# Optimization experiments

Hardware: AMD Instinct MI355X
Metric: run time of the kernel (lower is better)

The kernel has to match this reference:

```python
import jax, jax.numpy as jnp
import numpy as np

BETA = 0.2


def setup_inputs() -> dict:
    key = jax.random.key(0)
    ks = jax.random.split(key, 9)
    B, IN, W, OUT = 1024, 256, 512, 1
    def init_w(k, o, i):
        # torch.nn.Linear default: U(-1/sqrt(in), 1/sqrt(in))
        bound = 1.0 / np.sqrt(i)
        return jax.random.uniform(k, (o, i), jnp.float32, -bound, bound)
    def init_b(k, o, i):
        bound = 1.0 / np.sqrt(i)
        return jax.random.uniform(k, (o,), jnp.float32, -bound, bound)
    return {
        "x":  jax.random.normal(ks[0], (B, IN), jnp.float32),
        "W1": init_w(ks[1], W, IN),  "b1": init_b(ks[2], W, IN),
        "W2": init_w(ks[3], W, W),   "b2": init_b(ks[4], W, W),
        "W3": init_w(ks[5], W, W),   "b3": init_b(ks[6], W, W),
        "W4": init_w(ks[7], OUT, W), "b4": init_b(ks[8], OUT, W),
    }


def _max_tempered_out(x, W, b, beta=BETA):
    # lineared: standard linear part, (B, out)
    lin = jnp.einsum('oi,bi->bo', W, x)
    # tropical part: max over input dim of elementwise weight*input, (B, out)
    mx = jnp.max(W[None, :, :] * x[:, None, :], axis=-1)
    return (1.0 - beta) * lin + beta * mx + b


def reference(x, W1, b1, W2, b2, W3, b3, W4, b4):
    h = _max_tempered_out(x, W1, b1)
    h = _max_tempered_out(h, W2, b2)
    h = _max_tempered_out(h, W3, b3)
    out = _max_tempered_out(h, W4, b4)
    return jnp.squeeze(out, axis=-1)  # output_width == 1 -> (B,)
```

## Files before the change

kernel.cpp:

```cpp
#include <hip/hip_runtime.h>
#include <math.h>


#define NT   512
#define ROWS 4

#define WT1_OFF 0
#define WT2_OFF 33280
#define WT3_OFF 99328

__global__ __launch_bounds__(256) void transpose_all(
    const float* __restrict__ W1, const float* __restrict__ W2,
    const float* __restrict__ W3, float4* __restrict__ ws)
{
    const int tid = blockIdx.x * 256 + threadIdx.x;
    const float* W;
    float4* WT;
    int o, k4, K;
    if (tid < 32768) {
        W = W1; WT = ws + WT1_OFF; K = 256;
        o = tid >> 6; k4 = tid & 63;
    } else if (tid < 98304) {
        const int idx = tid - 32768;
        W = W2; WT = ws + WT2_OFF; K = 512;
        o = idx >> 7; k4 = idx & 127;
    } else {
        const int idx = tid - 98304;
        W = W3; WT = ws + WT3_OFF; K = 512;
        o = idx >> 7; k4 = idx & 127;
    }
    float4 v = *(const float4*)&W[(size_t)o * K + 4 * k4];
    WT[(size_t)k4 * 512 + o] = v;
}

__device__ __forceinline__ void layer_bcast(
    const float (*__restrict__ hin)[512],
    float (*__restrict__ hout)[512],
    const float4* __restrict__ WT,
    const float* __restrict__ bias,
    int K4, int t)
{
    float sa[ROWS], sb[ROWS], ma[ROWS], mb[ROWS];
    #pragma unroll
    for (int r = 0; r < ROWS; ++r) {
        sa[r] = 0.f; sb[r] = 0.f;
        ma[r] = -INFINITY; mb[r] = -INFINITY;
    }

    const float4* wp = WT + t;
    float4 w0 = wp[0];
    float4 w1 = wp[512];
    float4 w2 = wp[1024];
    float4 w3 = wp[1536];

    for (int kg = 0; kg < K4; kg += 4) {
        float4 n0 = w0, n1 = w1, n2 = w2, n3 = w3;
        if (kg + 4 < K4) {
            const float4* q = wp + (size_t)(kg + 4) * 512;
            n0 = q[0];
            n1 = q[512];
            n2 = q[1024];
            n3 = q[1536];
        }
        #pragma unroll
        for (int j = 0; j < 4; ++j) {
            const float4 w = (j == 0) ? w0 : (j == 1) ? w1 : (j == 2) ? w2 : w3;
            const int k = (kg + j) * 4;
            #pragma unroll
            for (int r = 0; r < ROWS; ++r) {
                float4 h = *(const float4*)&hin[r][k];
                float p;
                p = w.x * h.x; sa[r] += p; ma[r] = fmaxf(ma[r], p);
                p = w.y * h.y; sb[r] += p; mb[r] = fmaxf(mb[r], p);
                p = w.z * h.z; sa[r] += p; ma[r] = fmaxf(ma[r], p);
                p = w.w * h.w; sb[r] += p; mb[r] = fmaxf(mb[r], p);
            }
        }
        w0 = n0; w1 = n1; w2 = n2; w3 = n3;
    }

    const float bo = bias[t];
    #pragma unroll
    for (int r = 0; r < ROWS; ++r) {
        float s = sa[r] + sb[r];
        float m = fmaxf(ma[r], mb[r]);
        hout[r][t] = fmaf(0.2f, m, fmaf(0.8f, s, bo));
    }
}

__global__ __launch_bounds__(NT) void net_fused(
    const float* __restrict__ x,
    const float4* __restrict__ WT1, const float* __restrict__ b1,
    const float4* __restrict__ WT2, const float* __restrict__ b2,
    const float4* __restrict__ WT3, const float* __restrict__ b3,
    const float* __restrict__ W4,   const float* __restrict__ b4,
    float* __restrict__ out)
{
    __shared__ __align__(16) float ha[ROWS][512];
    __shared__ __align__(16) float hb[ROWS][512];
    __shared__ float red_s[8][ROWS];
    __shared__ float red_m[8][ROWS];

    const int t = threadIdx.x;
    const int row0 = blockIdx.x * ROWS;

    {
        const int r = t >> 7;
        const int c = (t & 127) * 2;
        float2 v = *(const float2*)&x[(size_t)(row0 + r) * 256 + c];
        ha[r][c]     = v.x;
        ha[r][c + 1] = v.y;
    }
    __syncthreads();

    layer_bcast(ha, hb, WT1, b1, 64,  t);
    __syncthreads();
    layer_bcast(hb, ha, WT2, b2, 128, t);
    __syncthreads();
    layer_bcast(ha, hb, WT3, b3, 128, t);
    __syncthreads();

    const float w4 = W4[t];
    float ps[ROWS], pm[ROWS];
    #pragma unroll
    for (int r = 0; r < ROWS; ++r) {
        float p = w4 * hb[r][t];
        ps[r] = p;
        pm[r] = p;
    }
    #pragma unroll
    for (int off = 32; off; off >>= 1) {
        #pragma unroll
        for (int r = 0; r < ROWS; ++r) {
            ps[r] += __shfl_xor(ps[r], off, 64);
            pm[r] = fmaxf(pm[r], __shfl_xor(pm[r], off, 64));
        }
    }
    const int lane = t & 63;
    const int wave = t >> 6;
    if (lane == 0) {
        #pragma unroll
        for (int r = 0; r < ROWS; ++r) {
            red_s[wave][r] = ps[r];
            red_m[wave][r] = pm[r];
        }
    }
    __syncthreads();

    if (t < ROWS) {
        float s = red_s[0][t];
        float m = red_m[0][t];
        #pragma unroll
        for (int w = 1; w < 8; ++w) {
            s += red_s[w][t];
            m = fmaxf(m, red_m[w][t]);
        }
        out[row0 + t] = fmaf(0.2f, m, fmaf(0.8f, s, b4[0]));
    }
}

extern "C" void kernel_launch(void* const* d_in, const int* in_sizes, int n_in,
                              void* d_out, int out_size, void* d_ws, size_t ws_size,
                              hipStream_t stream)
{
    const float* x  = (const float*)d_in[0];
    const float* W1 = (const float*)d_in[1];
    const float* b1 = (const float*)d_in[2];
    const float* W2 = (const float*)d_in[3];
    const float* b2 = (const float*)d_in[4];
    const float* W3 = (const float*)d_in[5];
    const float* b3 = (const float*)d_in[6];
    const float* W4 = (const float*)d_in[7];
    const float* b4 = (const float*)d_in[8];

    float4* ws4 = (float4*)d_ws;

    transpose_all<<<640, 256, 0, stream>>>(W1, W2, W3, ws4);

    net_fused<<<256, NT, 0, stream>>>(
        x,
        ws4 + WT1_OFF, b1,
        ws4 + WT2_OFF, b2,
        ws4 + WT3_OFF, b3,
        W4, b4,
        (float*)d_out);
}
```

Measured before the change: 66.27 us.

## Deepen weight prefetch, software-pipeline LDS loads, use packed FP32 math

New measurement: 183.9 us. 177% more time.

```diff
diff --git a/kernel.cpp b/kernel.cpp
--- a/kernel.cpp
+++ b/kernel.cpp
@@ -4,6 +4,8 @@
 
 #define NT   512
 #define ROWS 4
+
+typedef float v2f __attribute__((ext_vector_type(2)));
 
 #define WT1_OFF 0
 #define WT2_OFF 33280
@@ -33,62 +35,94 @@
     WT[(size_t)k4 * 512 + o] = v;
 }
 
+#define COMPUTE_K4(wv, H)                                                   \
+    {                                                                       \
+        v2f w01; w01[0] = (wv).x; w01[1] = (wv).y;                          \
+        v2f w23; w23[0] = (wv).z; w23[1] = (wv).w;                          \
+        _Pragma("unroll")                                                   \
+        for (int r = 0; r < ROWS; ++r) {                                    \
+            v2f h01; h01[0] = H[r].x; h01[1] = H[r].y;                      \
+            v2f h23; h23[0] = H[r].z; h23[1] = H[r].w;                      \
+            v2f p01 = w01 * h01;                                            \
+            v2f p23 = w23 * h23;                                            \
+            sA[r] += p01;                                                   \
+            sB[r] += p23;                                                   \
+            mA[r] = fmaxf(fmaxf(mA[r], p01[0]), p01[1]);                    \
+            mB[r] = fmaxf(fmaxf(mB[r], p23[0]), p23[1]);                    \
+        }                                                                   \
+    }
+
+#define LOADH(H, k4idx)                                                     \
+    {                                                                       \
+        _Pragma("unroll")                                                   \
+        for (int r = 0; r < ROWS; ++r)                                      \
+            H[r] = *(const float4*)&hin[r][(k4idx) * 4];                    \
+    }
+
+template<int K4>
 __device__ __forceinline__ void layer_bcast(
     const float (*__restrict__ hin)[512],
     float (*__restrict__ hout)[512],
     const float4* __restrict__ WT,
     const float* __restrict__ bias,
-    int K4, int t)
-{
-    float sa[ROWS], sb[ROWS], ma[ROWS], mb[ROWS];
+    int t)
+{
+    v2f sA[ROWS], sB[ROWS];
+    float mA[ROWS], mB[ROWS];
     #pragma unroll
     for (int r = 0; r < ROWS; ++r) {
-        sa[r] = 0.f; sb[r] = 0.f;
-        ma[r] = -INFINITY; mb[r] = -INFINITY;
+        sA[r] = (v2f)0.f; sB[r] = (v2f)0.f;
+        mA[r] = -INFINITY; mB[r] = -INFINITY;
     }
 
     const float4* wp = WT + t;
-    float4 w0 = wp[0];
-    float4 w1 = wp[512];
-    float4 w2 = wp[1024];
-    float4 w3 = wp[1536];
-
+
+    float4 wreg[8];
+    #pragma unroll
+    for (int i = 0; i < 8; ++i) wreg[i] = wp[(size_t)i * 512];
+
+    float4 hP0[ROWS], hP1[ROWS], hP2[ROWS], hP3[ROWS];
+    LOADH(hP0, 0); LOADH(hP1, 1); LOADH(hP2, 2); LOADH(hP3, 3);
+
+    #pragma unroll 1
     for (int kg = 0; kg < K4; kg += 4) {
-        float4 n0 = w0, n1 = w1, n2 = w2, n3 = w3;
-        if (kg + 4 < K4) {
-            const float4* q = wp + (size_t)(kg + 4) * 512;
-            n0 = q[0];
-            n1 = q[512];
-            n2 = q[1024];
-            n3 = q[1536];
-        }
-        #pragma unroll
-        for (int j = 0; j < 4; ++j) {
-            const float4 w = (j == 0) ? w0 : (j == 1) ? w1 : (j == 2) ? w2 : w3;
-            const int k = (kg + j) * 4;
-            #pragma unroll
-            for (int r = 0; r < ROWS; ++r) {
-                float4 h = *(const float4*)&hin[r][k];
-                float p;
-                p = w.x * h.x; sa[r] += p; ma[r] = fmaxf(ma[r], p);
-                p = w.y * h.y; sb[r] += p; mb[r] = fmaxf(mb[r], p);
-                p = w.z * h.z; sa[r] += p; ma[r] = fmaxf(ma[r], p);
-                p = w.w * h.w; sb[r] += p; mb[r] = fmaxf(mb[r], p);
-            }
-        }
-        w0 = n0; w1 = n1; w2 = n2; w3 = n3;
+        {
+            float4 wv = wreg[kg & 7];
+            if (kg + 8 < K4) wreg[kg & 7] = wp[(size_t)(kg + 8) * 512];
+            COMPUTE_K4(wv, hP0);
+            if (kg + 4 < K4) LOADH(hP0, kg + 4);
+        }
+        {
+            float4 wv = wreg[(kg + 1) & 7];
+            if (kg + 9 < K4) wreg[(kg + 1) & 7] = wp[(size_t)(kg + 9) * 512];
+            COMPUTE_K4(wv, hP1);
+            if (kg + 5 < K4) LOADH(hP1, kg + 5);
+        }
+        {
+            float4 wv = wreg[(kg + 2) & 7];
+            if (kg + 10 < K4) wreg[(kg + 2) & 7] = wp[(size_t)(kg + 10) * 512];
+            COMPUTE_K4(wv, hP2);
+            if (kg + 6 < K4) LOADH(hP2, kg + 6);
+        }
+        {
+            float4 wv = wreg[(kg + 3) & 7];
+            if (kg + 11 < K4) wreg[(kg + 3) & 7] = wp[(size_t)(kg + 11) * 512];
+            COMPUTE_K4(wv, hP3);
+            if (kg + 7 < K4) LOADH(hP3, kg + 7);
+        }
     }
 
     const float bo = bias[t];
     #pragma unroll
     for (int r = 0; r < ROWS; ++r) {
-        float s = sa[r] + sb[r];
-        float m = fmaxf(ma[r], mb[r]);
+        v2f sv = sA[r] + sB[r];
+        float s = sv[0] + sv[1];
+        float m = fmaxf(mA[r], mB[r]);
         hout[r][t] = fmaf(0.2f, m, fmaf(0.8f, s, bo));
     }
 }
 
-__global__ __launch_bounds__(NT) void net_fused(
+__global__ __launch_bounds__(NT, 2) void net_fused(
     const float* __restrict__ x,
     const float4* __restrict__ WT1, const float* __restrict__ b1,
     const float4* __restrict__ WT2, const float* __restrict__ b2,
@@ -113,11 +147,11 @@
     }
     __syncthreads();
 
-    layer_bcast(ha, hb, WT1, b1, 64,  t);
-    __syncthreads();
-    layer_bcast(hb, ha, WT2, b2, 128, t);
-    __syncthreads();
-    layer_bcast(ha, hb, WT3, b3, 128, t);
+    layer_bcast<64> (ha, hb, WT1, b1, t);
+    __syncthreads();
+    layer_bcast<128>(hb, ha, WT2, b2, t);
+    __syncthreads();
+    layer_bcast<128>(ha, hb, WT3, b3, t);
     __syncthreads();
 
     const float w4 = W4[t];
```

## Split K across thread halves with two outputs per thread and packed FP32 math

Applied to the files above, without the earlier changes.

Result: faster. 61.35 us (-7.4%).

```diff
diff --git a/kernel.cpp b/kernel.cpp
--- a/kernel.cpp
+++ b/kernel.cpp
@@ -3,7 +3,8 @@
 
 
 #define NT   512
-#define ROWS 4
+
+typedef float v2f __attribute__((ext_vector_type(2)));
 
 #define WT1_OFF 0
 #define WT2_OFF 33280
@@ -33,59 +34,100 @@
     WT[(size_t)k4 * 512 + o] = v;
 }
 
-__device__ __forceinline__ void layer_bcast(
+#define PROD(S, M, W01, W23, H01, H23)                                      \
+    {                                                                       \
+        v2f p = (W01) * (H01);                                              \
+        S += p; M = fmaxf(fmaxf(M, p[0]), p[1]);                            \
+        p = (W23) * (H23);                                                  \
+        S += p; M = fmaxf(fmaxf(M, p[0]), p[1]);                            \
+    }
+
+__device__ __forceinline__ void layer_split(
     const float (*__restrict__ hin)[512],
     float (*__restrict__ hout)[512],
     const float4* __restrict__ WT,
     const float* __restrict__ bias,
+    float4* __restrict__ scr,
     int K4, int t)
 {
-    float sa[ROWS], sb[ROWS], ma[ROWS], mb[ROWS];
+    const int o0   = t & 255;
+    const int half = t >> 8;
+    const int o1   = o0 + 256;
+    const int K4h  = K4 >> 1;
+
+    v2f s0[4], s1[4];
+    float m0[4], m1[4];
     #pragma unroll
-    for (int r = 0; r < ROWS; ++r) {
-        sa[r] = 0.f; sb[r] = 0.f;
-        ma[r] = -INFINITY; mb[r] = -INFINITY;
-    }
-
-    const float4* wp = WT + t;
-    float4 w0 = wp[0];
-    float4 w1 = wp[512];
-    float4 w2 = wp[1024];
-    float4 w3 = wp[1536];
-
-    for (int kg = 0; kg < K4; kg += 4) {
-        float4 n0 = w0, n1 = w1, n2 = w2, n3 = w3;
-        if (kg + 4 < K4) {
-            const float4* q = wp + (size_t)(kg + 4) * 512;
-            n0 = q[0];
-            n1 = q[512];
-            n2 = q[1024];
-            n3 = q[1536];
+    for (int r = 0; r < 4; ++r) {
+        s0[r] = (v2f)0.f; s1[r] = (v2f)0.f;
+        m0[r] = -INFINITY; m1[r] = -INFINITY;
+    }
+
+    const float4* wp0 = WT + (size_t)(half * K4h) * 512 + o0;
+    const float4* wp1 = wp0 + 256;
+    const float4* h0p = (const float4*)hin[0] + half * K4h;
+    const float4* h1p = (const float4*)hin[1] + half * K4h;
+    const float4* h2p = (const float4*)hin[2] + half * K4h;
+    const float4* h3p = (const float4*)hin[3] + half * K4h;
+
+    float4 u0 = wp0[0], u1 = wp0[512], u2 = wp0[1024], u3 = wp0[1536];
+    float4 v0 = wp1[0], v1 = wp1[512], v2 = wp1[1024], v3 = wp1[1536];
+
+    for (int kg = 0; kg < K4h; kg += 4) {
+        float4 nu0 = u0, nu1 = u1, nu2 = u2, nu3 = u3;
+        float4 nv0 = v0, nv1 = v1, nv2 = v2, nv3 = v3;
+        if (kg + 4 < K4h) {
+            const float4* q0 = wp0 + (size_t)(kg + 4) * 512;
+            const float4* q1 = wp1 + (size_t)(kg + 4) * 512;
+            nu0 = q0[0]; nu1 = q0[512]; nu2 = q0[1024]; nu3 = q0[1536];
+            nv0 = q1[0]; nv1 = q1[512]; nv2 = q1[1024]; nv3 = q1[1536];
         }
         #pragma unroll
         for (int j = 0; j < 4; ++j) {
-            const float4 w = (j == 0) ? w0 : (j == 1) ? w1 : (j == 2) ? w2 : w3;
-            const int k = (kg + j) * 4;
+            const float4 wu = (j == 0) ? u0 : (j == 1) ? u1 : (j == 2) ? u2 : u3;
+            const float4 wv = (j == 0) ? v0 : (j == 1) ? v1 : (j == 2) ? v2 : v3;
+            const int q = kg + j;
+            v2f u01; u01[0] = wu.x; u01[1] = wu.y;
+            v2f u23; u23[0] = wu.z; u23[1] = wu.w;
+            v2f w01; w01[0] = wv.x; w01[1] = wv.y;
+            v2f w23; w23[0] = wv.z; w23[1] = wv.w;
             #pragma unroll
-            for (int r = 0; r < ROWS; ++r) {
-                float4 h = *(const float4*)&hin[r][k];
-                float p;
-                p = w.x * h.x; sa[r] += p; ma[r] = fmaxf(ma[r], p);
-                p = w.y * h.y; sb[r] += p; mb[r] = fmaxf(mb[r], p);
-                p = w.z * h.z; sa[r] += p; ma[r] = fmaxf(ma[r], p);
-                p = w.w * h.w; sb[r] += p; mb[r] = fmaxf(mb[r], p);
+            for (int r = 0; r < 4; ++r) {
+                const float4 h = (r == 0) ? h0p[q] : (r == 1) ? h1p[q]
+                               : (r == 2) ? h2p[q] : h3p[q];
+                v2f h01; h01[0] = h.x; h01[1] = h.y;
+                v2f h23; h23[0] = h.z; h23[1] = h.w;
+                PROD(s0[r], m0[r], u01, u23, h01, h23);
+                PROD(s1[r], m1[r], w01, w23, h01, h23);
             }
         }
-        w0 = n0; w1 = n1; w2 = n2; w3 = n3;
-    }
-
+        u0 = nu0; u1 = nu1; u2 = nu2; u3 = nu3;
+        v0 = nv0; v1 = nv1; v2 = nv2; v3 = nv3;
+    }
+
+    float4 ps0, pm0, ps1, pm1;
+    ps0.x = s0[0][0] + s0[0][1]; ps0.y = s0[1][0] + s0[1][1];
+    ps0.z = s0[2][0] + s0[2][1]; ps0.w = s0[3][0] + s0[3][1];
+    ps1.x = s1[0][0] + s1[0][1]; ps1.y = s1[1][0] + s1[1][1];
+    ps1.z = s1[2][0] + s1[2][1]; ps1.w = s1[3][0] + s1[3][1];
+    pm0.x = m0[0]; pm0.y = m0[1]; pm0.z = m0[2]; pm0.w = m0[3];
+    pm1.x = m1[0]; pm1.y = m1[1]; pm1.z = m1[2]; pm1.w = m1[3];
+
+    scr[o0 * 2 + half]        = ps0;
+    scr[o1 * 2 + half]        = ps1;
+    scr[1024 + o0 * 2 + half] = pm0;
+    scr[1024 + o1 * 2 + half] = pm1;
+    __syncthreads();
+
+    const float4 sa = scr[t * 2 + 0];
+    const float4 sb = scr[t * 2 + 1];
+    const float4 ma = scr[1024 + t * 2 + 0];
+    const float4 mb = scr[1024 + t * 2 + 1];
     const float bo = bias[t];
-    #pragma unroll
-    for (int r = 0; r < ROWS; ++r) {
-        float s = sa[r] + sb[r];
-        float m = fmaxf(ma[r], mb[r]);
-        hout[r][t] = fmaf(0.2f, m, fmaf(0.8f, s, bo));
-    }
+    hout[0][t] = fmaf(0.2f, fmaxf(ma.x, mb.x), fmaf(0.8f, sa.x + sb.x, bo));
+    hout[1][t] = fmaf(0.2f, fmaxf(ma.y, mb.y), fmaf(0.8f, sa.y + sb.y, bo));
+    hout[2][t] = fmaf(0.2f, fmaxf(ma.z, mb.z), fmaf(0.8f, sa.z + sb.z, bo));
+    hout[3][t] = fmaf(0.2f, fmaxf(ma.w, mb.w), fmaf(0.8f, sa.w + sb.w, bo));
 }
 
 __global__ __launch_bounds__(NT) void net_fused(
@@ -96,13 +138,14 @@
     const float* __restrict__ W4,   const float* __restrict__ b4,
     float* __restrict__ out)
 {
-    __shared__ __align__(16) float ha[ROWS][512];
-    __shared__ __align__(16) float hb[ROWS][512];
-    __shared__ float red_s[8][ROWS];
-    __shared__ float red_m[8][ROWS];
+    __shared__ __align__(16) float ha[4][512];
+    __shared__ __align__(16) float hb[4][512];
+    __shared__ __align__(16) float4 scr[2048];
+    __shared__ float red_s[8][4];
+    __shared__ float red_m[8][4];
 
     const int t = threadIdx.x;
-    const int row0 = blockIdx.x * ROWS;
+    const int row0 = blockIdx.x * 4;
 
     {
         const int r = t >> 7;
@@ -113,41 +156,43 @@
     }
     __syncthreads();
 
-    layer_bcast(ha, hb, WT1, b1, 64,  t);
-    __syncthreads();
-    layer_bcast(hb, ha, WT2, b2, 128, t);
-    __syncthreads();
-    layer_bcast(ha, hb, WT3, b3, 128, t);
+    layer_split(ha, hb, WT1, b1, scr, 64,  t);
+    __syncthreads();
+    layer_split(hb, ha, WT2, b2, scr, 128, t);
+    __syncthreads();
+    layer_split(ha, hb, WT3, b3, scr, 128, t);
     __syncthreads();
 
     const float w4 = W4[t];
-    float ps[ROWS], pm[ROWS];
-    #pragma unroll
-    for (int r = 0; r < ROWS; ++r) {
-        float p = w4 * hb[r][t];
-        ps[r] = p;
-        pm[r] = p;
+    float ps0, ps1, ps2, ps3, pm0, pm1, pm2, pm3;
+    {
+        float p0 = w4 * hb[0][t]; ps0 = p0; pm0 = p0;
+        float p1 = w4 * hb[1][t]; ps1 = p1; pm1 = p1;
+        float p2 = w4 * hb[2][t]; ps2 = p2; pm2 = p2;
+        float p3 = w4 * hb[3][t]; ps3 = p3; pm3 = p3;
     }
     #pragma unroll
     for (int off = 32; off; off >>= 1) {
-        #pragma unroll
-        for (int r = 0; r < ROWS; ++r) {
-            ps[r] += __shfl_xor(ps[r], off, 64);
-            pm[r] = fmaxf(pm[r], __shfl_xor(pm[r], off, 64));
-        }
+        ps0 += __shfl_xor(ps0, off, 64);
+        pm0 = fmaxf(pm0, __shfl_xor(pm0, off, 64));
+        ps1 += __shfl_xor(ps1, off, 64);
+        pm1 = fmaxf(pm1, __shfl_xor(pm1, off, 64));
+        ps2 += __shfl_xor(ps2, off, 64);
+        pm2 = fmaxf(pm2, __shfl_xor(pm2, off, 64));
+        ps3 += __shfl_xor(ps3, off, 64);
+        pm3 = fmaxf(pm3, __shfl_xor(pm3, off, 64));
     }
     const int lane = t & 63;
     const int wave = t >> 6;
     if (lane == 0) {
-        #pragma unroll
-        for (int r = 0; r < ROWS; ++r) {
-            red_s[wave][r] = ps[r];
-            red_m[wave][r] = pm[r];
-        }
-    }
-    __syncthreads();
-
-    if (t < ROWS) {
+        red_s[wave][0] = ps0; red_m[wave][0] = pm0;
+        red_s[wave][1] = ps1; red_m[wave][1] = pm1;
+        red_s[wave][2] = ps2; red_m[wave][2] = pm2;
+        red_s[wave][3] = ps3; red_m[wave][3] = pm3;
+    }
+    __syncthreads();
+
+    if (t < 4) {
         float s = red_s[0][t];
         float m = red_m[0][t];
         #pragma unroll
```
